# Performance work log

Measured on AMD Instinct MI355X. Metric: run time of the kernel, lower is better.

The kernel has to match this reference:

```python
import jax, jax.numpy as jnp
import numpy as np

B, N, FIN, D = 4, 16384, 128, 256
GX, GY = 32, 32
M = GX * GY
NBR = 1
K = (2 * NBR + 1) ** 2
IMG_W, IMG_H = 256.0, 256.0
CELL_W, CELL_H = IMG_W / GX, IMG_H / GY
EPS = 1e-5

# (K,2) offsets, row-major (-n,-n)..(n,n), [dx,dy] like torch _build_offsets_2d
_ys, _xs = np.meshgrid(np.arange(-NBR, NBR + 1), np.arange(-NBR, NBR + 1), indexing='ij')
OFFSETS = jnp.asarray(np.stack([_xs.ravel(), _ys.ravel()], axis=-1), dtype=jnp.int32)  # (K,2)


def setup_inputs() -> dict:
    key = jax.random.key(0)
    ks = jax.random.split(key, 16)
    s = 0.02
    return {
        'features': jax.random.normal(ks[0], (B, N, FIN), dtype=jnp.float32),
        'coords': jax.random.uniform(ks[1], (B, N, 2), dtype=jnp.float32) * IMG_W,
        'valid_mask': jnp.ones((B, N), dtype=bool),
        'Wf': jax.random.normal(ks[2], (FIN, D), dtype=jnp.float32) * s,
        'bf': jnp.zeros((D,), dtype=jnp.float32),
        'Wq': jax.random.normal(ks[3], (D, D), dtype=jnp.float32) * s,
        'bq': jnp.zeros((D,), dtype=jnp.float32),
        'Wk': jax.random.normal(ks[4], (D, D), dtype=jnp.float32) * s,
        'bk': jnp.zeros((D,), dtype=jnp.float32),
        'Wv': jax.random.normal(ks[5], (D, D), dtype=jnp.float32) * s,
        'bv': jnp.zeros((D,), dtype=jnp.float32),
        'Wo': jax.random.normal(ks[6], (D, D), dtype=jnp.float32) * s,
        'bo': jnp.zeros((D,), dtype=jnp.float32),
        'pos_emb': jax.random.normal(ks[7], (K, D), dtype=jnp.float32) * s,
        'gamma': jnp.ones((D,), dtype=jnp.float32),
        'beta': jnp.zeros((D,), dtype=jnp.float32),
    }


def _forward(features, coords, valid_mask, Wf, bf, Wq, bq, Wk, bk, Wv, bv, Wo, bo, pos_emb, gamma, beta):
    feat = features @ Wf + bf  # (B,N,D)

    # coords -> grid cell indices (truncation == torch .long() for nonneg coords)
    ix = jnp.clip((coords[..., 0] / CELL_W).astype(jnp.int32), 0, GX - 1)
    iy = jnp.clip((coords[..., 1] / CELL_H).astype(jnp.int32), 0, GY - 1)
    lin = ix * GY + iy  # (B,N)

    # scatter-mean pool into grid cells
    base = (jnp.arange(B, dtype=jnp.int32) * M)[:, None]
    gid = (lin + base).reshape(-1)  # (B*N,)
    pooled = jax.ops.segment_sum(feat.reshape(-1, D), gid, num_segments=B * M)
    cnt = jax.ops.segment_sum(jnp.ones((B * N,), feat.dtype), gid, num_segments=B * M)
    grid_flat = (pooled / jnp.maximum(cnt, 1.0)[:, None]).reshape(B, M, D)

    # neighbor gather with edge clamping + validity mask
    nbx = ix[:, :, None] + OFFSETS[None, None, :, 0]  # (B,N,K)
    nby = iy[:, :, None] + OFFSETS[None, None, :, 1]
    valid = (nbx >= 0) & (nbx < GX) & (nby >= 0) & (nby < GY)
    lin_n = jnp.clip(nbx, 0, GX - 1) * GY + jnp.clip(nby, 0, GY - 1)  # (B,N,K)
    nbr_feat = jnp.take_along_axis(grid_flat, lin_n.reshape(B, N * K, 1), axis=1).reshape(B, N, K, D)
    nbr_feat = nbr_feat + pos_emb[None, None, :, :]

    # tiny-window attention (1 query vs K neighbors); SDPA scale = 1/sqrt(D)
    Q = feat @ Wq + bq  # (B,N,D)
    Kt = nbr_feat @ Wk + bk  # (B,N,K,D)
    Vt = nbr_feat @ Wv + bv
    scores = jnp.einsum('bnd,bnkd->bnk', Q, Kt) / jnp.sqrt(jnp.float32(D))
    scores = jnp.where(valid, scores, -jnp.inf)
    attn = jax.nn.softmax(scores, axis=-1)
    out = jnp.einsum('bnk,bnkd->bnd', attn, Vt)
    out = out @ Wo + bo

    # residual + layernorm
    h = feat + out
    mu = jnp.mean(h, axis=-1, keepdims=True)
    var = jnp.var(h, axis=-1, keepdims=True)
    h = (h - mu) * jax.lax.rsqrt(var + EPS) * gamma + beta

    return jnp.where(valid_mask[..., None], h, feat)


def reference(features, coords, valid_mask, Wf, bf, Wq, bq, Wk, bk, Wv, bv, Wo, bo, pos_emb, gamma, beta):
    return _forward(features, coords, valid_mask, Wf, bf, Wq, bq, Wk, bk, Wv, bv, Wo, bo, pos_emb, gamma, beta)
```

## Files before the change

kernel.cpp:

```cpp
#include <hip/hip_runtime.h>
#include <math.h>

typedef _Float16 f16;
typedef _Float16 f16x8 __attribute__((ext_vector_type(8)));
typedef float f32x4 __attribute__((ext_vector_type(4)));

constexpr int cB   = 4;
constexpr int cN   = 16384;
constexpr int cFIN = 128;
constexpr int cD   = 256;
constexpr int cGX  = 32;
constexpr int cGY  = 32;
constexpr int cM   = cGX * cGY;
constexpr int cBM  = cB * cM;
constexpr int cBN  = cB * cN;
constexpr int cK   = 9;
constexpr float cEPS = 1e-5f;
constexpr int RPB  = 64;

struct f16pair { f16 h; f16 l; };
__device__ inline f16pair split2(float x) {
  f16pair p;
  p.h = (f16)x;
  p.l = (f16)(x - (float)p.h);
  return p;
}

__global__ __launch_bounds__(256)
void k_index(const float* __restrict__ coords, int* __restrict__ lin_arr,
             int* __restrict__ cntI) {
  int p = blockIdx.x * 256 + threadIdx.x;
  if (p >= cBN) return;
  float x = coords[2 * p], y = coords[2 * p + 1];
  int ix = (int)(x * 0.125f);
  int iy = (int)(y * 0.125f);
  ix = min(max(ix, 0), cGX - 1);
  iy = min(max(iy, 0), cGY - 1);
  int lin = ix * cGY + iy;
  lin_arr[p] = lin;
  int b = p / cN;
  atomicAdd(&cntI[b * cM + lin], 1);
}

__global__ __launch_bounds__(1024)
void k_scan(const int* __restrict__ cntI, int* __restrict__ bstart) {
  __shared__ int sums[1024];
  int t = threadIdx.x;
  int base = t * 4;
  int v0 = cntI[base], v1 = cntI[base + 1], v2 = cntI[base + 2], v3 = cntI[base + 3];
  sums[t] = v0 + v1 + v2 + v3;
  __syncthreads();
  for (int off = 1; off < 1024; off <<= 1) {
    int val = (t >= off) ? sums[t - off] : 0;
    __syncthreads();
    sums[t] += val;
    __syncthreads();
  }
  int run = (t == 0) ? 0 : sums[t - 1];
  bstart[base] = run; run += v0;
  bstart[base + 1] = run; run += v1;
  bstart[base + 2] = run; run += v2;
  bstart[base + 3] = run; run += v3;
  if (t == 1023) bstart[4096] = run;
}

__global__ __launch_bounds__(256)
void k_scatteridx(const int* __restrict__ lin_arr, const int* __restrict__ bstart,
                  int* __restrict__ bfill, int* __restrict__ sorted) {
  int p = blockIdx.x * 256 + threadIdx.x;
  if (p >= cBN) return;
  int b = p / cN;
  int gid = b * cM + lin_arr[p];
  int pos = bstart[gid] + atomicAdd(&bfill[gid], 1);
  sorted[pos] = p;
}

__global__ __launch_bounds__(256)
void k_convertA(const float* __restrict__ features, f16* __restrict__ Ah,
                f16* __restrict__ Al) {
  int i = blockIdx.x * 256 + threadIdx.x;
  const float4* src = (const float4*)features;
  float4 a = src[2 * i], b = src[2 * i + 1];
  f16x8 oh, ol;
  f16pair p0 = split2(a.x), p1 = split2(a.y), p2 = split2(a.z), p3 = split2(a.w);
  f16pair p4 = split2(b.x), p5 = split2(b.y), p6 = split2(b.z), p7 = split2(b.w);
  oh[0] = p0.h; ol[0] = p0.l; oh[1] = p1.h; ol[1] = p1.l;
  oh[2] = p2.h; ol[2] = p2.l; oh[3] = p3.h; ol[3] = p3.l;
  oh[4] = p4.h; ol[4] = p4.l; oh[5] = p5.h; ol[5] = p5.l;
  oh[6] = p6.h; ol[6] = p6.l; oh[7] = p7.h; ol[7] = p7.l;
  ((f16x8*)Ah)[i] = oh;
  ((f16x8*)Al)[i] = ol;
}

__global__ __launch_bounds__(256)
void k_convertWf(const float* __restrict__ Wf, f16* __restrict__ WfTh,
                 f16* __restrict__ WfTl) {
  int i = blockIdx.x * 256 + threadIdx.x;
  int n = i >> 7, k = i & 127;
  f16pair p = split2(Wf[k * cD + n]);
  WfTh[i] = p.h; WfTl[i] = p.l;
}

__global__ __launch_bounds__(256)
void k_precompute(const float* __restrict__ Wf, const float* __restrict__ Wq,
                  const float* __restrict__ Wv, const float* __restrict__ Wo,
                  const float* __restrict__ bf, const float* __restrict__ bq,
                  const float* __restrict__ bv, const float* __restrict__ bo,
                  f16* __restrict__ WfqTh, f16* __restrict__ WfqTl,
                  float* __restrict__ Wvo, float* __restrict__ bq2,
                  float* __restrict__ bvo) {
  int bid = blockIdx.x, n = threadIdx.x;
  if (bid < cFIN) {
    int k = bid;
    float acc = 0.f;
    for (int c = 0; c < cD; c++) acc += Wf[k * cD + c] * Wq[c * cD + n];
    f16pair p = split2(acc);
    WfqTh[n * cFIN + k] = p.h;
    WfqTl[n * cFIN + k] = p.l;
  } else if (bid < cFIN + cD) {
    int k = bid - cFIN;
    float acc = 0.f;
    for (int c = 0; c < cD; c++) acc += Wv[k * cD + c] * Wo[c * cD + n];
    Wvo[k * cD + n] = acc;
  } else {
    float aq = 0.f, ao = 0.f;
    for (int c = 0; c < cD; c++) {
      aq += bf[c] * Wq[c * cD + n];
      ao += bv[c] * Wo[c * cD + n];
    }
    bq2[n] = aq + bq[n];
    bvo[n] = ao + bo[n];
  }
}

constexpr int CPB = 8;
__global__ __launch_bounds__(256)
void k_pool_gemm(const float* __restrict__ features, const int* __restrict__ sorted,
                 const int* __restrict__ bstart,
                 const float* __restrict__ Wf, const float* __restrict__ bf,
                 const float* __restrict__ Wk, const float* __restrict__ Wvo,
                 float* __restrict__ GK, float* __restrict__ GVO) {
  __shared__ float Ssum[CPB][cFIN];
  __shared__ float Stmp[2][cFIN];
  __shared__ float gsh[CPB][cD];
  int t = threadIdx.x;
  int cell0 = blockIdx.x * CPB;
  int half = t >> 7, ch = t & 127;

  for (int j = 0; j < CPB; j++) {
    int gid = cell0 + j;
    int s0 = bstart[gid], s1 = bstart[gid + 1];
    float acc = 0.f;
    for (int i = s0 + half; i < s1; i += 2)
      acc += features[(size_t)sorted[i] * cFIN + ch];
    Stmp[half][ch] = acc;
    __syncthreads();
    if (half == 0) Ssum[j][ch] = Stmp[0][ch] + Stmp[1][ch];
    __syncthreads();
  }

  float accG[CPB];
#pragma unroll
  for (int j = 0; j < CPB; j++) accG[j] = 0.f;
  for (int c4 = 0; c4 < cFIN / 4; c4++) {
    float w0 = Wf[(4 * c4 + 0) * cD + t];
    float w1 = Wf[(4 * c4 + 1) * cD + t];
    float w2 = Wf[(4 * c4 + 2) * cD + t];
    float w3 = Wf[(4 * c4 + 3) * cD + t];
#pragma unroll
    for (int j = 0; j < CPB; j++) {
      float4 a = *(const float4*)&Ssum[j][4 * c4];
      accG[j] += a.x * w0 + a.y * w1 + a.z * w2 + a.w * w3;
    }
  }
  float bfv = bf[t];
  for (int j = 0; j < CPB; j++) {
    int gid = cell0 + j;
    int cnt = bstart[gid + 1] - bstart[gid];
    gsh[j][t] = (cnt > 0) ? (accG[j] / (float)cnt + bfv) : 0.f;
  }
  __syncthreads();

  float accK[CPB], accV[CPB];
#pragma unroll
  for (int j = 0; j < CPB; j++) { accK[j] = 0.f; accV[j] = 0.f; }
  for (int c4 = 0; c4 < cD / 4; c4++) {
    float k0 = Wk[(4 * c4 + 0) * cD + t];
    float k1 = Wk[(4 * c4 + 1) * cD + t];
    float k2 = Wk[(4 * c4 + 2) * cD + t];
    float k3 = Wk[(4 * c4 + 3) * cD + t];
    float v0 = Wvo[(4 * c4 + 0) * cD + t];
    float v1 = Wvo[(4 * c4 + 1) * cD + t];
    float v2 = Wvo[(4 * c4 + 2) * cD + t];
    float v3 = Wvo[(4 * c4 + 3) * cD + t];
#pragma unroll
    for (int j = 0; j < CPB; j++) {
      float4 g = *(const float4*)&gsh[j][4 * c4];
      accK[j] += g.x * k0 + g.y * k1 + g.z * k2 + g.w * k3;
      accV[j] += g.x * v0 + g.y * v1 + g.z * v2 + g.w * v3;
    }
  }
  for (int j = 0; j < CPB; j++) {
    GK[(size_t)(cell0 + j) * cD + t] = accK[j];
    GVO[(size_t)(cell0 + j) * cD + t] = accV[j];
  }
}

__global__ __launch_bounds__(256)
void k_posemb(const float* __restrict__ pe, const float* __restrict__ Wk,
              const float* __restrict__ bk, const float* __restrict__ Wvo,
              float* __restrict__ PK, float* __restrict__ PVO) {
  __shared__ float p[cD];
  int k = blockIdx.x, t = threadIdx.x;
  p[t] = pe[k * cD + t];
  __syncthreads();
  float ak = 0.f, av = 0.f;
  for (int c = 0; c < cD; c++) {
    float pv = p[c];
    ak += pv * Wk[c * cD + t];
    av += pv * Wvo[c * cD + t];
  }
  PK[k * cD + t] = ak + bk[t];
  PVO[k * cD + t] = av;
}

__global__ __launch_bounds__(256)
void k_gemmAB(const f16* __restrict__ Ah, const f16* __restrict__ Al,
              const f16* __restrict__ BTh0, const f16* __restrict__ BTl0,
              const float* __restrict__ bias0, float* __restrict__ out0,
              const f16* __restrict__ BTh1, const f16* __restrict__ BTl1,
              const float* __restrict__ bias1, float* __restrict__ out1) {
  const f16* BTh = blockIdx.y ? BTh1 : BTh0;
  const f16* BTl = blockIdx.y ? BTl1 : BTl0;
  const float* bias = blockIdx.y ? bias1 : bias0;
  float* outp = blockIdx.y ? out1 : out0;
  int t = threadIdx.x;
  int w = t >> 6, lane = t & 63;
  int q = lane >> 4, l = lane & 15;
  size_t row0 = (size_t)blockIdx.x * RPB;

  f32x4 acc[4][4];
#pragma unroll
  for (int rs = 0; rs < 4; rs++)
#pragma unroll
    for (int tc = 0; tc < 4; tc++) acc[rs][tc] = (f32x4){0.f, 0.f, 0.f, 0.f};

  for (int kk = 0; kk < cFIN; kk += 32) {
    f16x8 a_h[4], a_l[4];
#pragma unroll
    for (int rs = 0; rs < 4; rs++) {
      size_t aoff = (row0 + rs * 16 + l) * cFIN + q * 8 + kk;
      a_h[rs] = *(const f16x8*)(Ah + aoff);
      a_l[rs] = *(const f16x8*)(Al + aoff);
    }
#pragma unroll
    for (int tc = 0; tc < 4; tc++) {
      size_t boff = (size_t)((w * 4 + tc) * 16 + l) * cFIN + q * 8 + kk;
      f16x8 bh = *(const f16x8*)(BTh + boff);
      f16x8 bl = *(const f16x8*)(BTl + boff);
#pragma unroll
      for (int rs = 0; rs < 4; rs++) {
        acc[rs][tc] = __builtin_amdgcn_mfma_f32_16x16x32_f16(a_h[rs], bh, acc[rs][tc], 0, 0, 0);
        acc[rs][tc] = __builtin_amdgcn_mfma_f32_16x16x32_f16(a_h[rs], bl, acc[rs][tc], 0, 0, 0);
        acc[rs][tc] = __builtin_amdgcn_mfma_f32_16x16x32_f16(a_l[rs], bh, acc[rs][tc], 0, 0, 0);
      }
    }
  }
#pragma unroll
  for (int tc = 0; tc < 4; tc++) {
    int col = (w * 4 + tc) * 16 + l;
    float b = bias[col];
#pragma unroll
    for (int rs = 0; rs < 4; rs++)
#pragma unroll
      for (int r = 0; r < 4; r++) {
        int lr = rs * 16 + q * 4 + r;
        outp[(row0 + lr) * cD + col] = acc[rs][tc][r] + b;
      }
  }
}

__global__ __launch_bounds__(256)
void k_attn(float* Qbuf, const float* __restrict__ GK,
            const float* __restrict__ GVO, const float* __restrict__ PK,
            const float* __restrict__ PVO, const int* __restrict__ sorted,
            const int* __restrict__ bstart) {
  __shared__ float KK[cK][cD];
  __shared__ float VV[cK][cD];
  int gid = blockIdx.x;
  int b = gid / cM;
  int lin = gid % cM;
  int ix = lin / cGY, iy = lin % cGY;
  int t = threadIdx.x;

  int vm = 0;
  for (int k = 0; k < cK; k++) {
    int dx = k % 3 - 1, dy = k / 3 - 1;
    int nx = ix + dx, ny = iy + dy;
    bool v = (nx >= 0 && nx < cGX && ny >= 0 && ny < cGY);
    if (v) vm |= (1 << k);
    int cx = min(max(nx, 0), cGX - 1);
    int cy = min(max(ny, 0), cGY - 1);
    size_t nlin = (size_t)(b * cM + cx * cGY + cy);
    KK[k][t] = GK[nlin * cD + t] + PK[k * cD + t];
    VV[k][t] = GVO[nlin * cD + t] + PVO[k * cD + t];
  }
  __syncthreads();

  int s0 = bstart[gid], s1 = bstart[gid + 1];
  int wv = t >> 6, lane = t & 63;
  for (int ip = s0 + wv; ip < s1; ip += 4) {
    int p = sorted[ip];
    float4 q4 = *(const float4*)&Qbuf[(size_t)p * cD + lane * 4];
    float sc[cK];
#pragma unroll
    for (int k = 0; k < cK; k++) {
      float4 kk = *(const float4*)&KK[k][lane * 4];
      sc[k] = q4.x * kk.x + q4.y * kk.y + q4.z * kk.z + q4.w * kk.w;
    }
#pragma unroll
    for (int off = 32; off > 0; off >>= 1)
#pragma unroll
      for (int k = 0; k < cK; k++) sc[k] += __shfl_xor(sc[k], off, 64);

    float mx = -1e30f;
#pragma unroll
    for (int k = 0; k < cK; k++)
      if ((vm >> k) & 1) mx = fmaxf(mx, sc[k] * 0.0625f);
    float e[cK], ssum = 0.f;
#pragma unroll
    for (int k = 0; k < cK; k++) {
      float v = ((vm >> k) & 1) ? __expf(sc[k] * 0.0625f - mx) : 0.f;
      e[k] = v; ssum += v;
    }
    float inv = 1.f / ssum;
    float4 o = {0.f, 0.f, 0.f, 0.f};
#pragma unroll
    for (int k = 0; k < cK; k++) {
      float a = e[k] * inv;
      float4 vv = *(const float4*)&VV[k][lane * 4];
      o.x += a * vv.x; o.y += a * vv.y; o.z += a * vv.z; o.w += a * vv.w;
    }
    *(float4*)&Qbuf[(size_t)p * cD + lane * 4] = o;
  }
}

__global__ __launch_bounds__(256)
void k_ln(const float* __restrict__ attn, const float* __restrict__ bvop,
          const float* __restrict__ gammap, const float* __restrict__ betap,
          float* __restrict__ out) {
  int t = threadIdx.x;
  int w = t >> 6, lane = t & 63;
  size_t row = (size_t)blockIdx.x * 4 + w;
  size_t off = row * cD + lane * 4;
  float4 a = *(const float4*)&attn[off];
  float4 f = *(const float4*)&out[off];
  float4 c = *(const float4*)&bvop[lane * 4];
  float4 h;
  h.x = f.x + a.x + c.x; h.y = f.y + a.y + c.y;
  h.z = f.z + a.z + c.z; h.w = f.w + a.w + c.w;
  float s = h.x + h.y + h.z + h.w;
  float ss = h.x * h.x + h.y * h.y + h.z * h.z + h.w * h.w;
#pragma unroll
  for (int o2 = 32; o2 > 0; o2 >>= 1) {
    s += __shfl_xor(s, o2, 64);
    ss += __shfl_xor(ss, o2, 64);
  }
  float mu = s * (1.f / cD);
  float var = ss * (1.f / cD) - mu * mu;
  float rs = rsqrtf(var + cEPS);
  float4 g = *(const float4*)&gammap[lane * 4];
  float4 be = *(const float4*)&betap[lane * 4];
  float4 o;
  o.x = (h.x - mu) * rs * g.x + be.x;
  o.y = (h.y - mu) * rs * g.y + be.y;
  o.z = (h.z - mu) * rs * g.z + be.z;
  o.w = (h.w - mu) * rs * g.w + be.w;
  *(float4*)&out[off] = o;
}

extern "C" void kernel_launch(void* const* d_in, const int* in_sizes, int n_in,
                              void* d_out, int out_size, void* d_ws, size_t ws_size,
                              hipStream_t stream) {
  (void)in_sizes; (void)n_in; (void)out_size; (void)ws_size;
  const float* features = (const float*)d_in[0];
  const float* coords   = (const float*)d_in[1];
  const float* Wf = (const float*)d_in[3];
  const float* bf = (const float*)d_in[4];
  const float* Wq = (const float*)d_in[5];
  const float* bq = (const float*)d_in[6];
  const float* Wk = (const float*)d_in[7];
  const float* bk = (const float*)d_in[8];
  const float* Wv = (const float*)d_in[9];
  const float* bv = (const float*)d_in[10];
  const float* Wo = (const float*)d_in[11];
  const float* bo = (const float*)d_in[12];
  const float* pe = (const float*)d_in[13];
  const float* gm = (const float*)d_in[14];
  const float* bt = (const float*)d_in[15];
  float* out = (float*)d_out;

  char* ws = (char*)d_ws;
  size_t o = 0;
  auto take = [&](size_t bytes) -> void* {
    void* p = ws + o;
    o = (o + bytes + 255) & ~(size_t)255;
    return p;
  };
  int* lin_arr = (int*)take((size_t)cBN * 4);
  int* sorted  = (int*)take((size_t)cBN * 4);
  int* bstart  = (int*)take((size_t)(cBM + 1) * 4);
  int* bfill   = (int*)take((size_t)cBM * 4);
  int* cntI    = (int*)take((size_t)cBM * 4);
  float* GK    = (float*)take((size_t)cBM * cD * 4);
  float* GVO   = (float*)take((size_t)cBM * cD * 4);
  float* PK    = (float*)take((size_t)cK * cD * 4);
  float* PVO   = (float*)take((size_t)cK * cD * 4);
  float* Qbuf  = (float*)take((size_t)cBN * cD * 4);
  f16* Afh     = (f16*)take((size_t)cBN * cFIN * 2);
  f16* Afl     = (f16*)take((size_t)cBN * cFIN * 2);
  f16* WfTh    = (f16*)take((size_t)cD * cFIN * 2);
  f16* WfTl    = (f16*)take((size_t)cD * cFIN * 2);
  f16* WfqTh   = (f16*)take((size_t)cD * cFIN * 2);
  f16* WfqTl   = (f16*)take((size_t)cD * cFIN * 2);
  float* Wvo   = (float*)take((size_t)cD * cD * 4);
  float* bq2   = (float*)take((size_t)cD * 4);
  float* bvo   = (float*)take((size_t)cD * 4);

  (void)hipMemsetAsync(cntI, 0, (size_t)cBM * 4, stream);
  (void)hipMemsetAsync(bfill, 0, (size_t)cBM * 4, stream);

  k_index<<<cBN / 256, 256, 0, stream>>>(coords, lin_arr, cntI);
  k_scan<<<1, 1024, 0, stream>>>(cntI, bstart);
  k_scatteridx<<<cBN / 256, 256, 0, stream>>>(lin_arr, bstart, bfill, sorted);
  k_convertA<<<cBN * cFIN / (256 * 8), 256, 0, stream>>>(features, Afh, Afl);
  k_convertWf<<<cD * cFIN / 256, 256, 0, stream>>>(Wf, WfTh, WfTl);
  k_precompute<<<cFIN + cD + 1, 256, 0, stream>>>(Wf, Wq, Wv, Wo, bf, bq, bv, bo,
                                                  WfqTh, WfqTl, Wvo, bq2, bvo);
  k_pool_gemm<<<cBM / CPB, 256, 0, stream>>>(features, sorted, bstart, Wf, bf, Wk, Wvo, GK, GVO);
  k_posemb<<<cK, 256, 0, stream>>>(pe, Wk, bk, Wvo, PK, PVO);
  dim3 gAB(cBN / RPB, 2);
  k_gemmAB<<<gAB, 256, 0, stream>>>(Afh, Afl, WfTh, WfTl, bf, out,
                                    WfqTh, WfqTl, bq2, Qbuf);
  k_attn<<<cBM, 256, 0, stream>>>(Qbuf, GK, GVO, PK, PVO, sorted, bstart);
  k_ln<<<cBN / 4, 256, 0, stream>>>(Qbuf, bvo, gm, bt, out);
}
```

Before: 374.2 us.

## Move grid-cell GEMMs to split-f16 MFMA and fuse layernorm into attention

Result: faster. 343.4 us (-8.2%).

```diff
diff --git a/kernel.cpp b/kernel.cpp
--- a/kernel.cpp
+++ b/kernel.cpp
@@ -104,11 +104,14 @@
 __global__ __launch_bounds__(256)
 void k_precompute(const float* __restrict__ Wf, const float* __restrict__ Wq,
                   const float* __restrict__ Wv, const float* __restrict__ Wo,
+                  const float* __restrict__ Wk,
                   const float* __restrict__ bf, const float* __restrict__ bq,
                   const float* __restrict__ bv, const float* __restrict__ bo,
                   f16* __restrict__ WfqTh, f16* __restrict__ WfqTl,
-                  float* __restrict__ Wvo, float* __restrict__ bq2,
-                  float* __restrict__ bvo) {
+                  float* __restrict__ Wvo,
+                  f16* __restrict__ WvoTh, f16* __restrict__ WvoTl,
+                  f16* __restrict__ WkTh, f16* __restrict__ WkTl,
+                  float* __restrict__ bq2, float* __restrict__ bvo) {
   int bid = blockIdx.x, n = threadIdx.x;
   if (bid < cFIN) {
     int k = bid;
@@ -122,7 +125,10 @@
     float acc = 0.f;
     for (int c = 0; c < cD; c++) acc += Wv[k * cD + c] * Wo[c * cD + n];
     Wvo[k * cD + n] = acc;
-  } else {
+    f16pair p = split2(acc);
+    WvoTh[n * cD + k] = p.h;
+    WvoTl[n * cD + k] = p.l;
+  } else if (bid == cFIN + cD) {
     float aq = 0.f, ao = 0.f;
     for (int c = 0; c < cD; c++) {
       aq += bf[c] * Wq[c * cD + n];
@@ -130,79 +136,141 @@
     }
     bq2[n] = aq + bq[n];
     bvo[n] = ao + bo[n];
-  }
-}
-
-constexpr int CPB = 8;
-__global__ __launch_bounds__(256)
-void k_pool_gemm(const float* __restrict__ features, const int* __restrict__ sorted,
-                 const int* __restrict__ bstart,
-                 const float* __restrict__ Wf, const float* __restrict__ bf,
-                 const float* __restrict__ Wk, const float* __restrict__ Wvo,
-                 float* __restrict__ GK, float* __restrict__ GVO) {
-  __shared__ float Ssum[CPB][cFIN];
+  } else {
+    int n2 = bid - (cFIN + cD + 1);
+    f16pair p = split2(Wk[n * cD + n2]);
+    WkTh[n2 * cD + n] = p.h;
+    WkTl[n2 * cD + n] = p.l;
+  }
+}
+
+__global__ __launch_bounds__(256)
+void k_poolsum(const float* __restrict__ features, const int* __restrict__ sorted,
+               const int* __restrict__ bstart, f16* __restrict__ Sh,
+               f16* __restrict__ Sl) {
   __shared__ float Stmp[2][cFIN];
-  __shared__ float gsh[CPB][cD];
+  int gid = blockIdx.x;
   int t = threadIdx.x;
-  int cell0 = blockIdx.x * CPB;
   int half = t >> 7, ch = t & 127;
-
-  for (int j = 0; j < CPB; j++) {
-    int gid = cell0 + j;
-    int s0 = bstart[gid], s1 = bstart[gid + 1];
-    float acc = 0.f;
-    for (int i = s0 + half; i < s1; i += 2)
-      acc += features[(size_t)sorted[i] * cFIN + ch];
-    Stmp[half][ch] = acc;
-    __syncthreads();
-    if (half == 0) Ssum[j][ch] = Stmp[0][ch] + Stmp[1][ch];
-    __syncthreads();
-  }
-
-  float accG[CPB];
-#pragma unroll
-  for (int j = 0; j < CPB; j++) accG[j] = 0.f;
-  for (int c4 = 0; c4 < cFIN / 4; c4++) {
-    float w0 = Wf[(4 * c4 + 0) * cD + t];
-    float w1 = Wf[(4 * c4 + 1) * cD + t];
-    float w2 = Wf[(4 * c4 + 2) * cD + t];
-    float w3 = Wf[(4 * c4 + 3) * cD + t];
-#pragma unroll
-    for (int j = 0; j < CPB; j++) {
-      float4 a = *(const float4*)&Ssum[j][4 * c4];
-      accG[j] += a.x * w0 + a.y * w1 + a.z * w2 + a.w * w3;
-    }
-  }
-  float bfv = bf[t];
-  for (int j = 0; j < CPB; j++) {
-    int gid = cell0 + j;
-    int cnt = bstart[gid + 1] - bstart[gid];
-    gsh[j][t] = (cnt > 0) ? (accG[j] / (float)cnt + bfv) : 0.f;
-  }
+  int s0 = bstart[gid], s1 = bstart[gid + 1];
+  float acc = 0.f;
+  for (int i = s0 + half; i < s1; i += 2)
+    acc += features[(size_t)sorted[i] * cFIN + ch];
+  Stmp[half][ch] = acc;
   __syncthreads();
-
-  float accK[CPB], accV[CPB];
-#pragma unroll
-  for (int j = 0; j < CPB; j++) { accK[j] = 0.f; accV[j] = 0.f; }
-  for (int c4 = 0; c4 < cD / 4; c4++) {
-    float k0 = Wk[(4 * c4 + 0) * cD + t];
-    float k1 = Wk[(4 * c4 + 1) * cD + t];
-    float k2 = Wk[(4 * c4 + 2) * cD + t];
-    float k3 = Wk[(4 * c4 + 3) * cD + t];
-    float v0 = Wvo[(4 * c4 + 0) * cD + t];
-    float v1 = Wvo[(4 * c4 + 1) * cD + t];
-    float v2 = Wvo[(4 * c4 + 2) * cD + t];
-    float v3 = Wvo[(4 * c4 + 3) * cD + t];
-#pragma unroll
-    for (int j = 0; j < CPB; j++) {
-      float4 g = *(const float4*)&gsh[j][4 * c4];
-      accK[j] += g.x * k0 + g.y * k1 + g.z * k2 + g.w * k3;
-      accV[j] += g.x * v0 + g.y * v1 + g.z * v2 + g.w * v3;
-    }
-  }
-  for (int j = 0; j < CPB; j++) {
-    GK[(size_t)(cell0 + j) * cD + t] = accK[j];
-    GVO[(size_t)(cell0 + j) * cD + t] = accV[j];
+  if (half == 0) {
+    f16pair p = split2(Stmp[0][ch] + Stmp[1][ch]);
+    Sh[(size_t)gid * cFIN + ch] = p.h;
+    Sl[(size_t)gid * cFIN + ch] = p.l;
+  }
+}
+
+__global__ __launch_bounds__(256)
+void k_gemm_g(const f16* __restrict__ Sh, const f16* __restrict__ Sl,
+              const f16* __restrict__ WfTh, const f16* __restrict__ WfTl,
+              const float* __restrict__ bfp, const int* __restrict__ bstart,
+              f16* __restrict__ Gh, f16* __restrict__ Gl) {
+  int t = threadIdx.x;
+  int w = t >> 6, lane = t & 63;
+  int q = lane >> 4, l = lane & 15;
+  size_t row0 = (size_t)blockIdx.x * RPB;
+
+  f32x4 acc[4][4];
+#pragma unroll
+  for (int rs = 0; rs < 4; rs++)
+#pragma unroll
+    for (int tc = 0; tc < 4; tc++) acc[rs][tc] = (f32x4){0.f, 0.f, 0.f, 0.f};
+
+  for (int kk = 0; kk < cFIN; kk += 32) {
+    f16x8 a_h[4], a_l[4];
+#pragma unroll
+    for (int rs = 0; rs < 4; rs++) {
+      size_t aoff = (row0 + rs * 16 + l) * cFIN + q * 8 + kk;
+      a_h[rs] = *(const f16x8*)(Sh + aoff);
+      a_l[rs] = *(const f16x8*)(Sl + aoff);
+    }
+#pragma unroll
+    for (int tc = 0; tc < 4; tc++) {
+      size_t boff = (size_t)((w * 4 + tc) * 16 + l) * cFIN + q * 8 + kk;
+      f16x8 bh = *(const f16x8*)(WfTh + boff);
+      f16x8 bl = *(const f16x8*)(WfTl + boff);
+#pragma unroll
+      for (int rs = 0; rs < 4; rs++) {
+        acc[rs][tc] = __builtin_amdgcn_mfma_f32_16x16x32_f16(a_h[rs], bh, acc[rs][tc], 0, 0, 0);
+        acc[rs][tc] = __builtin_amdgcn_mfma_f32_16x16x32_f16(a_h[rs], bl, acc[rs][tc], 0, 0, 0);
+        acc[rs][tc] = __builtin_amdgcn_mfma_f32_16x16x32_f16(a_l[rs], bh, acc[rs][tc], 0, 0, 0);
+      }
+    }
+  }
+#pragma unroll
+  for (int tc = 0; tc < 4; tc++) {
+    int col = (w * 4 + tc) * 16 + l;
+    float bias = bfp[col];
+#pragma unroll
+    for (int rs = 0; rs < 4; rs++)
+#pragma unroll
+      for (int r = 0; r < 4; r++) {
+        size_t row = row0 + rs * 16 + q * 4 + r;
+        int cnt = bstart[row + 1] - bstart[row];
+        float g = (cnt > 0) ? (acc[rs][tc][r] / (float)cnt + bias) : 0.f;
+        f16pair p = split2(g);
+        Gh[row * cD + col] = p.h;
+        Gl[row * cD + col] = p.l;
+      }
+  }
+}
+
+__global__ __launch_bounds__(256)
+void k_gemm_kv(const f16* __restrict__ Gh, const f16* __restrict__ Gl,
+               const f16* __restrict__ WkTh, const f16* __restrict__ WkTl,
+               float* __restrict__ GK,
+               const f16* __restrict__ WvoTh, const f16* __restrict__ WvoTl,
+               float* __restrict__ GVO) {
+  const f16* BTh = blockIdx.y ? WvoTh : WkTh;
+  const f16* BTl = blockIdx.y ? WvoTl : WkTl;
+  float* outp = blockIdx.y ? GVO : GK;
+  int t = threadIdx.x;
+  int w = t >> 6, lane = t & 63;
+  int q = lane >> 4, l = lane & 15;
+  size_t row0 = (size_t)blockIdx.x * RPB;
+
+  f32x4 acc[4][4];
+#pragma unroll
+  for (int rs = 0; rs < 4; rs++)
+#pragma unroll
+    for (int tc = 0; tc < 4; tc++) acc[rs][tc] = (f32x4){0.f, 0.f, 0.f, 0.f};
+
+  for (int kk = 0; kk < cD; kk += 32) {
+    f16x8 a_h[4], a_l[4];
+#pragma unroll
+    for (int rs = 0; rs < 4; rs++) {
+      size_t aoff = (row0 + rs * 16 + l) * cD + q * 8 + kk;
+      a_h[rs] = *(const f16x8*)(Gh + aoff);
+      a_l[rs] = *(const f16x8*)(Gl + aoff);
+    }
+#pragma unroll
+    for (int tc = 0; tc < 4; tc++) {
+      size_t boff = (size_t)((w * 4 + tc) * 16 + l) * cD + q * 8 + kk;
+      f16x8 bh = *(const f16x8*)(BTh + boff);
+      f16x8 bl = *(const f16x8*)(BTl + boff);
+#pragma unroll
+      for (int rs = 0; rs < 4; rs++) {
+        acc[rs][tc] = __builtin_amdgcn_mfma_f32_16x16x32_f16(a_h[rs], bh, acc[rs][tc], 0, 0, 0);
+        acc[rs][tc] = __builtin_amdgcn_mfma_f32_16x16x32_f16(a_h[rs], bl, acc[rs][tc], 0, 0, 0);
+        acc[rs][tc] = __builtin_amdgcn_mfma_f32_16x16x32_f16(a_l[rs], bh, acc[rs][tc], 0, 0, 0);
+      }
+    }
+  }
+#pragma unroll
+  for (int tc = 0; tc < 4; tc++) {
+    int col = (w * 4 + tc) * 16 + l;
+#pragma unroll
+    for (int rs = 0; rs < 4; rs++)
+#pragma unroll
+      for (int r = 0; r < 4; r++) {
+        size_t row = row0 + rs * 16 + q * 4 + r;
+        outp[row * cD + col] = acc[rs][tc][r];
+      }
   }
 }
 
@@ -281,10 +349,12 @@
 }
 
 __global__ __launch_bounds__(256)
-void k_attn(float* Qbuf, const float* __restrict__ GK,
+void k_attn(const float* __restrict__ Qbuf, const float* __restrict__ GK,
             const float* __restrict__ GVO, const float* __restrict__ PK,
             const float* __restrict__ PVO, const int* __restrict__ sorted,
-            const int* __restrict__ bstart) {
+            const int* __restrict__ bstart, const float* __restrict__ bvop,
+            const float* __restrict__ gammap, const float* __restrict__ betap,
+            float* __restrict__ out) {
   __shared__ float KK[cK][cD];
   __shared__ float VV[cK][cD];
   int gid = blockIdx.x;
@@ -309,6 +379,9 @@
 
   int s0 = bstart[gid], s1 = bstart[gid + 1];
   int wv = t >> 6, lane = t & 63;
+  float4 c4 = *(const float4*)&bvop[lane * 4];
+  float4 g4 = *(const float4*)&gammap[lane * 4];
+  float4 be4 = *(const float4*)&betap[lane * 4];
   for (int ip = s0 + wv; ip < s1; ip += 4) {
     int p = sorted[ip];
     float4 q4 = *(const float4*)&Qbuf[(size_t)p * cD + lane * 4];
@@ -341,42 +414,28 @@
       float4 vv = *(const float4*)&VV[k][lane * 4];
       o.x += a * vv.x; o.y += a * vv.y; o.z += a * vv.z; o.w += a * vv.w;
     }
-    *(float4*)&Qbuf[(size_t)p * cD + lane * 4] = o;
-  }
-}
-
-__global__ __launch_bounds__(256)
-void k_ln(const float* __restrict__ attn, const float* __restrict__ bvop,
-          const float* __restrict__ gammap, const float* __restrict__ betap,
-          float* __restrict__ out) {
-  int t = threadIdx.x;
-  int w = t >> 6, lane = t & 63;
-  size_t row = (size_t)blockIdx.x * 4 + w;
-  size_t off = row * cD + lane * 4;
-  float4 a = *(const float4*)&attn[off];
-  float4 f = *(const float4*)&out[off];
-  float4 c = *(const float4*)&bvop[lane * 4];
-  float4 h;
-  h.x = f.x + a.x + c.x; h.y = f.y + a.y + c.y;
-  h.z = f.z + a.z + c.z; h.w = f.w + a.w + c.w;
-  float s = h.x + h.y + h.z + h.w;
-  float ss = h.x * h.x + h.y * h.y + h.z * h.z + h.w * h.w;
-#pragma unroll
-  for (int o2 = 32; o2 > 0; o2 >>= 1) {
-    s += __shfl_xor(s, o2, 64);
-    ss += __shfl_xor(ss, o2, 64);
-  }
-  float mu = s * (1.f / cD);
-  float var = ss * (1.f / cD) - mu * mu;
-  float rs = rsqrtf(var + cEPS);
-  float4 g = *(const float4*)&gammap[lane * 4];
-  float4 be = *(const float4*)&betap[lane * 4];
-  float4 o;
-  o.x = (h.x - mu) * rs * g.x + be.x;
-  o.y = (h.y - mu) * rs * g.y + be.y;
-  o.z = (h.z - mu) * rs * g.z + be.z;
-  o.w = (h.w - mu) * rs * g.w + be.w;
-  *(float4*)&out[off] = o;
+    size_t off0 = (size_t)p * cD + lane * 4;
+    float4 f = *(const float4*)&out[off0];
+    float4 h;
+    h.x = f.x + o.x + c4.x; h.y = f.y + o.y + c4.y;
+    h.z = f.z + o.z + c4.z; h.w = f.w + o.w + c4.w;
+    float s = h.x + h.y + h.z + h.w;
+    float ss = h.x * h.x + h.y * h.y + h.z * h.z + h.w * h.w;
+#pragma unroll
+    for (int o2 = 32; o2 > 0; o2 >>= 1) {
+      s += __shfl_xor(s, o2, 64);
+      ss += __shfl_xor(ss, o2, 64);
+    }
+    float mu = s * (1.f / cD);
+    float var = ss * (1.f / cD) - mu * mu;
+    float rs = rsqrtf(var + cEPS);
+    float4 r;
+    r.x = (h.x - mu) * rs * g4.x + be4.x;
+    r.y = (h.y - mu) * rs * g4.y + be4.y;
+    r.z = (h.z - mu) * rs * g4.z + be4.z;
+    r.w = (h.w - mu) * rs * g4.w + be4.w;
+    *(float4*)&out[off0] = r;
+  }
 }
 
 extern "C" void kernel_launch(void* const* d_in, const int* in_sizes, int n_in,
@@ -424,6 +483,14 @@
   f16* WfqTh   = (f16*)take((size_t)cD * cFIN * 2);
   f16* WfqTl   = (f16*)take((size_t)cD * cFIN * 2);
   float* Wvo   = (float*)take((size_t)cD * cD * 4);
+  f16* WvoTh   = (f16*)take((size_t)cD * cD * 2);
+  f16* WvoTl   = (f16*)take((size_t)cD * cD * 2);
+  f16* WkTh    = (f16*)take((size_t)cD * cD * 2);
+  f16* WkTl    = (f16*)take((size_t)cD * cD * 2);
+  f16* Sh      = (f16*)take((size_t)cBM * cFIN * 2);
+  f16* Sl      = (f16*)take((size_t)cBM * cFIN * 2);
+  f16* Gh      = (f16*)take((size_t)cBM * cD * 2);
+  f16* Gl      = (f16*)take((size_t)cBM * cD * 2);
   float* bq2   = (float*)take((size_t)cD * 4);
   float* bvo   = (float*)take((size_t)cD * 4);
 
@@ -435,13 +502,17 @@
   k_scatteridx<<<cBN / 256, 256, 0, stream>>>(lin_arr, bstart, bfill, sorted);
   k_convertA<<<cBN * cFIN / (256 * 8), 256, 0, stream>>>(features, Afh, Afl);
   k_convertWf<<<cD * cFIN / 256, 256, 0, stream>>>(Wf, WfTh, WfTl);
-  k_precompute<<<cFIN + cD + 1, 256, 0, stream>>>(Wf, Wq, Wv, Wo, bf, bq, bv, bo,
-                                                  WfqTh, WfqTl, Wvo, bq2, bvo);
-  k_pool_gemm<<<cBM / CPB, 256, 0, stream>>>(features, sorted, bstart, Wf, bf, Wk, Wvo, GK, GVO);
+  k_precompute<<<cFIN + cD + 1 + cD, 256, 0, stream>>>(
+      Wf, Wq, Wv, Wo, Wk, bf, bq, bv, bo,
+      WfqTh, WfqTl, Wvo, WvoTh, WvoTl, WkTh, WkTl, bq2, bvo);
+  k_poolsum<<<cBM, 256, 0, stream>>>(features, sorted, bstart, Sh, Sl);
+  k_gemm_g<<<cBM / RPB, 256, 0, stream>>>(Sh, Sl, WfTh, WfTl, bf, bstart, Gh, Gl);
+  dim3 gKV(cBM / RPB, 2);
+  k_gemm_kv<<<gKV, 256, 0, stream>>>(Gh, Gl, WkTh, WkTl, GK, WvoTh, WvoTl, GVO);
   k_posemb<<<cK, 256, 0, stream>>>(pe, Wk, bk, Wvo, PK, PVO);
   dim3 gAB(cBN / RPB, 2);
   k_gemmAB<<<gAB, 256, 0, stream>>>(Afh, Afl, WfTh, WfTl, bf, out,
                                     WfqTh, WfqTl, bq2, Qbuf);
-  k_attn<<<cBM, 256, 0, stream>>>(Qbuf, GK, GVO, PK, PVO, sorted, bstart);
-  k_ln<<<cBN / 4, 256, 0, stream>>>(Qbuf, bvo, gm, bt, out);
-}
+  k_attn<<<cBM, 256, 0, stream>>>(Qbuf, GK, GVO, PK, PVO, sorted, bstart,
+                                  bvo, gm, bt, out);
+}
```
